# Kernel optimization log

Measured on AMD Instinct MI355X. Metric: run time of the kernel, lower is better.

Reference implementation:

```python
import jax, jax.numpy as jnp
import numpy as np

N_NODES = 100000
NEG_SLOPE = 0.2


def _gat_conv(x, edge_index, W, att_src, att_dst, bias):
    """Single-head PyG-style GATConv with self-loops.
    x: [N, F_in], edge_index: [2, E] (row 0 = src j, row 1 = dst i).
    """
    N = x.shape[0]
    h = x @ W  # [N, F_out]
    # add self-loops
    loop = jnp.arange(N, dtype=edge_index.dtype)
    src = jnp.concatenate([edge_index[0], loop])
    dst = jnp.concatenate([edge_index[1], loop])
    # per-node attention terms, gathered per edge
    a_s = h @ att_src  # [N]
    a_d = h @ att_dst  # [N]
    e = jax.nn.leaky_relu(a_s[src] + a_d[dst], NEG_SLOPE)  # [E+N]
    # segment softmax over incoming edges of each destination
    m = jax.ops.segment_max(e, dst, num_segments=N)  # [N]
    m = jnp.where(jnp.isfinite(m), m, 0.0)
    p = jnp.exp(e - m[dst])
    denom = jax.ops.segment_sum(p, dst, num_segments=N)  # [N], >0 due to self-loops
    alpha = p / denom[dst]  # [E+N]
    # scatter-aggregate weighted source features
    out = jax.ops.segment_sum(h[src] * alpha[:, None], dst, num_segments=N)
    return out + bias


def setup_inputs() -> dict:
    key = jax.random.key(0)
    ks = jax.random.split(key, 12)
    F_in, H, C = 128, 64, 40
    x = jax.random.normal(ks[0], (N_NODES, F_in), dtype=jnp.float32)
    edge_index = jax.random.randint(ks[1], (2, 1600000), 0, N_NODES, dtype=jnp.int64)
    s1 = 1.0 / np.sqrt(F_in)
    s2 = 1.0 / np.sqrt(H)
    return {
        "x": x,
        "edge_index": edge_index,
        "W1": jax.random.uniform(ks[2], (F_in, H), jnp.float32, -s1, s1),
        "att_src1": jax.random.uniform(ks[3], (H,), jnp.float32, -s2, s2),
        "att_dst1": jax.random.uniform(ks[4], (H,), jnp.float32, -s2, s2),
        "b1": jnp.zeros((H,), jnp.float32),
        "W2": jax.random.uniform(ks[5], (H, C), jnp.float32, -s2, s2),
        "att_src2": jax.random.uniform(ks[6], (C,), jnp.float32, -1.0 / np.sqrt(C), 1.0 / np.sqrt(C)),
        "att_dst2": jax.random.uniform(ks[7], (C,), jnp.float32, -1.0 / np.sqrt(C), 1.0 / np.sqrt(C)),
        "b2": jnp.zeros((C,), jnp.float32),
    }


def reference(x, edge_index, W1, att_src1, att_dst1, b1, W2, att_src2, att_dst2, b2):
    h = _gat_conv(x, edge_index, W1, att_src1, att_dst1, b1)
    h = jax.nn.relu(h)
    # dropout is identity in eval mode
    out = _gat_conv(h, edge_index, W2, att_src2, att_dst2, b2)
    return out
```

## Files before the change

### kernel.cpp

```cpp
#include <hip/hip_runtime.h>
#include <math.h>


#define NEG_SLOPE 0.2f
#define BIN_SHIFT 10
#define BIN_NODES 1024
#define MAXBINS   128
#define CAPB      17408
#define K1_CHUNK  4096
#define MAXDEG    128
#define AGG_STRIDE 132
#define XS_STRIDE 68

typedef _Float16 h4_t __attribute__((ext_vector_type(4)));

__device__ __forceinline__ float lrelu(float v) {
    return v > 0.f ? v : NEG_SLOPE * v;
}

__global__ __launch_bounds__(256) void bin_kernel(
    const int* __restrict__ src, const int* __restrict__ dst, int E, int nbins,
    int* __restrict__ bin_cursor, int* __restrict__ binned)
{
    __shared__ int hist[MAXBINS];
    __shared__ int base[MAXBINS];
    __shared__ int lcur[MAXBINS];
    const int tid = threadIdx.x;
    const int e0 = blockIdx.x * K1_CHUNK;

    if (tid < nbins) hist[tid] = 0;
    __syncthreads();

    for (int k = tid; k < K1_CHUNK; k += 256) {
        int e = e0 + k;
        if (e < E) atomicAdd(&hist[dst[e] >> BIN_SHIFT], 1);
    }
    __syncthreads();

    if (tid < nbins) {
        int c = hist[tid];
        base[tid] = (c > 0) ? atomicAdd(&bin_cursor[tid], c) : 0;
        lcur[tid] = 0;
    }
    __syncthreads();

    for (int k = tid; k < K1_CHUNK; k += 256) {
        int e = e0 + k;
        if (e < E) {
            int d = dst[e];
            int s = src[e];
            int b = d >> BIN_SHIFT;
            int o = atomicAdd(&lcur[b], 1);
            int pos = base[b] + o;
            if (pos < CAPB)
                binned[b * CAPB + pos] = (s << BIN_SHIFT) | (d & (BIN_NODES - 1));
        }
    }
}

__global__ __launch_bounds__(128) void scan_kernel(
    const int* __restrict__ bin_cursor, int* __restrict__ bin_base, int nbins)
{
    __shared__ int a[MAXBINS];
    const int tid = threadIdx.x;
    int v = (tid < nbins) ? min(bin_cursor[tid], CAPB) : 0;
    a[tid] = v;
    __syncthreads();
#pragma unroll
    for (int ofs = 1; ofs < 128; ofs <<= 1) {
        int t = (tid >= ofs) ? a[tid - ofs] : 0;
        __syncthreads();
        a[tid] += t;
        __syncthreads();
    }
    if (tid < nbins) bin_base[tid] = a[tid] - v;
}

__global__ __launch_bounds__(1024) void fine_kernel(
    const int* __restrict__ bin_cursor, const int* __restrict__ bin_base,
    const int* __restrict__ binned,
    int* __restrict__ csr, int* __restrict__ rowptr, int N, int nbins)
{
    __shared__ int a[BIN_NODES];
    __shared__ int cur[BIN_NODES];
    const int b = blockIdx.x;
    const int tid = threadIdx.x;

    const int cnt = min(bin_cursor[b], CAPB);
    const int binbase = bin_base[b];
    const int nn = min(BIN_NODES, N - b * BIN_NODES);
    const int* __restrict__ brec = binned + (long)b * CAPB;

    a[tid] = 0;
    __syncthreads();

    for (int k = tid; k < cnt; k += 1024) {
        atomicAdd(&a[brec[k] & (BIN_NODES - 1)], 1);
    }
    __syncthreads();

    int v = a[tid];
#pragma unroll
    for (int ofs = 1; ofs < BIN_NODES; ofs <<= 1) {
        int t = (tid >= ofs) ? a[tid - ofs] : 0;
        __syncthreads();
        a[tid] += t;
        __syncthreads();
    }
    const int excl = a[tid] - v;

    if (tid < nn) rowptr[b * BIN_NODES + tid] = binbase + excl;
    cur[tid] = binbase + excl;
    if (b == nbins - 1 && tid == 0) rowptr[N] = binbase + cnt;
    __syncthreads();

    for (int k = tid; k < cnt; k += 1024) {
        int rec = brec[k];
        int pos = atomicAdd(&cur[rec & (BIN_NODES - 1)], 1);
        csr[pos] = rec >> BIN_SHIFT;
    }
}

__global__ __launch_bounds__(256) void gemm1_kernel(
    const float* __restrict__ x, const float* __restrict__ W,
    const float* __restrict__ att_s, const float* __restrict__ att_d,
    _Float16* __restrict__ h, float* __restrict__ as_, float* __restrict__ ad_,
    int N)
{
    __shared__ float Ws[64 * 64];
    __shared__ float Xs[64 * XS_STRIDE];
    const int tid = threadIdx.x;
    const int cx = tid & 15;
    const int ry = tid >> 4;
    const long rowbase = (long)blockIdx.x * 64;
    const long gmax = (long)N * 32;

    float4 acc[4];
#pragma unroll
    for (int r = 0; r < 4; ++r) acc[r] = make_float4(0.f, 0.f, 0.f, 0.f);

    for (int kc = 0; kc < 2; ++kc) {
        __syncthreads();
        {
            const float4* W4 = (const float4*)W;
            float4* Ws4 = (float4*)Ws;
#pragma unroll
            for (int i = 0; i < 4; ++i)
                Ws4[tid + i * 256] = W4[kc * 1024 + tid + i * 256];
        }
        {
            const float4* X4 = (const float4*)x;
#pragma unroll
            for (int i = 0; i < 4; ++i) {
                int f = tid + i * 256;
                int row = f >> 4, c4 = f & 15;
                long gi = (rowbase + row) * 32 + kc * 16 + c4;
                float4 v = (gi < gmax) ? X4[gi] : make_float4(0.f, 0.f, 0.f, 0.f);
                *(float4*)&Xs[row * XS_STRIDE + c4 * 4] = v;
            }
        }
        __syncthreads();

#pragma unroll 4
        for (int k = 0; k < 64; k += 4) {
            float4 w0 = *(const float4*)&Ws[(k + 0) * 64 + cx * 4];
            float4 w1 = *(const float4*)&Ws[(k + 1) * 64 + cx * 4];
            float4 w2 = *(const float4*)&Ws[(k + 2) * 64 + cx * 4];
            float4 w3 = *(const float4*)&Ws[(k + 3) * 64 + cx * 4];
#pragma unroll
            for (int r = 0; r < 4; ++r) {
                float4 xv = *(const float4*)&Xs[(ry * 4 + r) * XS_STRIDE + k];
                acc[r].x += xv.x * w0.x + xv.y * w1.x + xv.z * w2.x + xv.w * w3.x;
                acc[r].y += xv.x * w0.y + xv.y * w1.y + xv.z * w2.y + xv.w * w3.y;
                acc[r].z += xv.x * w0.z + xv.y * w1.z + xv.z * w2.z + xv.w * w3.z;
                acc[r].w += xv.x * w0.w + xv.y * w1.w + xv.z * w2.w + xv.w * w3.w;
            }
        }
    }

    const float4 s4 = ((const float4*)att_s)[cx];
    const float4 d4 = ((const float4*)att_d)[cx];
#pragma unroll
    for (int r = 0; r < 4; ++r) {
        float ps = acc[r].x * s4.x + acc[r].y * s4.y + acc[r].z * s4.z + acc[r].w * s4.w;
        float pd = acc[r].x * d4.x + acc[r].y * d4.y + acc[r].z * d4.z + acc[r].w * d4.w;
#pragma unroll
        for (int off = 1; off < 16; off <<= 1) {
            ps += __shfl_xor(ps, off);
            pd += __shfl_xor(pd, off);
        }
        const long row = rowbase + ry * 4 + r;
        if (row < N) {
            h4_t hv;
            hv.x = (_Float16)acc[r].x; hv.y = (_Float16)acc[r].y;
            hv.z = (_Float16)acc[r].z; hv.w = (_Float16)acc[r].w;
            *(h4_t*)&h[row * 64 + cx * 4] = hv;
            if (cx == 0) { as_[row] = ps; ad_[row] = pd; }
        }
    }
}

__global__ __launch_bounds__(256) void gemm2_kernel(
    const float* __restrict__ hin, const float* __restrict__ W,
    const float* __restrict__ att_s, const float* __restrict__ att_d,
    _Float16* __restrict__ h2, float* __restrict__ as_, float* __restrict__ ad_,
    int N)
{
    __shared__ float Ws[64 * 40];
    __shared__ float Xs[64 * XS_STRIDE];
    const int tid = threadIdx.x;
    const int cx = tid & 15;
    const int ry = tid >> 4;
    const long rowbase = (long)blockIdx.x * 64;
    const bool act = (cx < 10);
    const int cq = act ? cx * 4 : 0;

    {
        const float4* W4 = (const float4*)W;
        float4* Ws4 = (float4*)Ws;
        Ws4[tid] = W4[tid];
        Ws4[tid + 256] = W4[tid + 256];
        if (tid < 128) Ws4[tid + 512] = W4[tid + 512];
    }
    {
        const float4* X4 = (const float4*)hin;
        const long gmax = (long)N * 16;
#pragma unroll
        for (int i = 0; i < 4; ++i) {
            int f = tid + i * 256;
            int row = f >> 4, c4 = f & 15;
            long gi = (rowbase + row) * 16 + c4;
            float4 v = (gi < gmax) ? X4[gi] : make_float4(0.f, 0.f, 0.f, 0.f);
            v.x = fmaxf(v.x, 0.f); v.y = fmaxf(v.y, 0.f);
            v.z = fmaxf(v.z, 0.f); v.w = fmaxf(v.w, 0.f);
            *(float4*)&Xs[row * XS_STRIDE + c4 * 4] = v;
        }
    }
    __syncthreads();

    float4 acc[4];
#pragma unroll
    for (int r = 0; r < 4; ++r) acc[r] = make_float4(0.f, 0.f, 0.f, 0.f);

#pragma unroll 4
    for (int k = 0; k < 64; k += 4) {
        float4 w0 = *(const float4*)&Ws[(k + 0) * 40 + cq];
        float4 w1 = *(const float4*)&Ws[(k + 1) * 40 + cq];
        float4 w2 = *(const float4*)&Ws[(k + 2) * 40 + cq];
        float4 w3 = *(const float4*)&Ws[(k + 3) * 40 + cq];
#pragma unroll
        for (int r = 0; r < 4; ++r) {
            float4 xv = *(const float4*)&Xs[(ry * 4 + r) * XS_STRIDE + k];
            acc[r].x += xv.x * w0.x + xv.y * w1.x + xv.z * w2.x + xv.w * w3.x;
            acc[r].y += xv.x * w0.y + xv.y * w1.y + xv.z * w2.y + xv.w * w3.y;
            acc[r].z += xv.x * w0.z + xv.y * w1.z + xv.z * w2.z + xv.w * w3.z;
            acc[r].w += xv.x * w0.w + xv.y * w1.w + xv.z * w2.w + xv.w * w3.w;
        }
    }

    const float4 s4 = act ? ((const float4*)att_s)[cx] : make_float4(0.f,0.f,0.f,0.f);
    const float4 d4 = act ? ((const float4*)att_d)[cx] : make_float4(0.f,0.f,0.f,0.f);
#pragma unroll
    for (int r = 0; r < 4; ++r) {
        float ps = act ? (acc[r].x * s4.x + acc[r].y * s4.y + acc[r].z * s4.z + acc[r].w * s4.w) : 0.f;
        float pd = act ? (acc[r].x * d4.x + acc[r].y * d4.y + acc[r].z * d4.z + acc[r].w * d4.w) : 0.f;
#pragma unroll
        for (int off = 1; off < 16; off <<= 1) {
            ps += __shfl_xor(ps, off);
            pd += __shfl_xor(pd, off);
        }
        const long row = rowbase + ry * 4 + r;
        if (row < N) {
            if (act) {
                h4_t hv;
                hv.x = (_Float16)acc[r].x; hv.y = (_Float16)acc[r].y;
                hv.z = (_Float16)acc[r].z; hv.w = (_Float16)acc[r].w;
                *(h4_t*)&h2[row * 40 + cq] = hv;
            }
            if (cx == 0) { as_[row] = ps; ad_[row] = pd; }
        }
    }
}

template<int F>
__global__ __launch_bounds__(256) void aggregate_kernel(
    const _Float16* __restrict__ h, const float* __restrict__ as_,
    const float* __restrict__ ad_, const int* __restrict__ rowptr,
    const int* __restrict__ csr, const float* __restrict__ bias,
    float* __restrict__ out, int N)
{
    __shared__ int   Ss[16 * AGG_STRIDE];
    __shared__ float Ps[16 * AGG_STRIDE];
    const int tid = threadIdx.x;
    const int dl  = tid >> 4;
    const int sub = tid & 15;
    const int i = blockIdx.x * 16 + dl;
    const bool alive = (i < N);

    int r0 = 0, deg = 0;
    if (alive) {
        r0 = rowptr[i];
        deg = rowptr[i + 1] - r0;
        if (deg > MAXDEG) deg = MAXDEG;
    }
    const float adi    = alive ? ad_[i] : 0.f;
    const float e_self = alive ? lrelu(as_[i] + adi) : 0.f;

    int*   __restrict__ sp = &Ss[dl * AGG_STRIDE];
    float* __restrict__ pp = &Ps[dl * AGG_STRIDE];

    float psum = 0.f;
    for (int c = sub; c < deg; c += 16) {
        int s = csr[r0 + c];
        float p = __expf(lrelu(as_[s] + adi));
        sp[c] = s;
        pp[c] = p;
        psum += p;
    }
#pragma unroll
    for (int off = 1; off < 16; off <<= 1) psum += __shfl_xor(psum, off);
    const float p_self = __expf(e_self);
    const float inv = 1.f / (psum + p_self);

    const bool act = (sub * 4 < F);
    const int  col = act ? sub * 4 : 0;
    float4 acc = make_float4(0.f, 0.f, 0.f, 0.f);

    int k = 0;
    for (; k + 4 <= deg; k += 4) {
        int   sA = sp[k],     sB = sp[k + 1], sC = sp[k + 2], sD = sp[k + 3];
        float pA = pp[k],     pB = pp[k + 1], pC = pp[k + 2], pD = pp[k + 3];
        if (act) {
            h4_t hA = *(const h4_t*)&h[(long)sA * F + col];
            h4_t hB = *(const h4_t*)&h[(long)sB * F + col];
            h4_t hC = *(const h4_t*)&h[(long)sC * F + col];
            h4_t hD = *(const h4_t*)&h[(long)sD * F + col];
            acc.x += (float)hA.x * pA + (float)hB.x * pB + (float)hC.x * pC + (float)hD.x * pD;
            acc.y += (float)hA.y * pA + (float)hB.y * pB + (float)hC.y * pC + (float)hD.y * pD;
            acc.z += (float)hA.z * pA + (float)hB.z * pB + (float)hC.z * pC + (float)hD.z * pD;
            acc.w += (float)hA.w * pA + (float)hB.w * pB + (float)hC.w * pC + (float)hD.w * pD;
        }
    }
    for (; k < deg; ++k) {
        int   s = sp[k];
        float p = pp[k];
        if (act) {
            h4_t hv = *(const h4_t*)&h[(long)s * F + col];
            acc.x += (float)hv.x * p; acc.y += (float)hv.y * p;
            acc.z += (float)hv.z * p; acc.w += (float)hv.w * p;
        }
    }

    if (alive && act) {
        h4_t hv = *(const h4_t*)&h[(long)i * F + col];
        float4 bv = *(const float4*)&bias[col];
        float4 o;
        o.x = (acc.x + (float)hv.x * p_self) * inv + bv.x;
        o.y = (acc.y + (float)hv.y * p_self) * inv + bv.y;
        o.z = (acc.z + (float)hv.z * p_self) * inv + bv.z;
        o.w = (acc.w + (float)hv.w * p_self) * inv + bv.w;
        *(float4*)&out[(long)i * F + col] = o;
    }
}

extern "C" void kernel_launch(void* const* d_in, const int* in_sizes, int n_in,
                              void* d_out, int out_size, void* d_ws, size_t ws_size,
                              hipStream_t stream) {
    const float* x    = (const float*)d_in[0];
    const int*   ei   = (const int*)d_in[1];
    const float* W1   = (const float*)d_in[2];
    const float* at_s1= (const float*)d_in[3];
    const float* at_d1= (const float*)d_in[4];
    const float* b1   = (const float*)d_in[5];
    const float* W2   = (const float*)d_in[6];
    const float* at_s2= (const float*)d_in[7];
    const float* at_d2= (const float*)d_in[8];
    const float* b2   = (const float*)d_in[9];
    float* out = (float*)d_out;

    const int N = in_sizes[0] / 128;
    const int E = in_sizes[1] / 2;
    const int nbins = (N + BIN_NODES - 1) >> BIN_SHIFT;

    char* p = (char*)d_ws;
    auto carve = [&](size_t bytes) -> void* {
        void* r = (void*)p;
        p += (bytes + 255) & ~(size_t)255;
        return r;
    };
    int*       bin_cursor = (int*)      carve((size_t)MAXBINS * 4);
    int*       bin_base   = (int*)      carve((size_t)MAXBINS * 4);
    int*       binned     = (int*)      carve((size_t)nbins * CAPB * 4);
    int*       csr        = (int*)      carve((size_t)E * 4);
    int*       rowptr     = (int*)      carve((size_t)(N + 1) * 4);
    _Float16*  h1         = (_Float16*) carve((size_t)N * 64 * 2);
    float*     agg1       = (float*)    carve((size_t)N * 64 * 4);
    _Float16*  h2         = (_Float16*) carve((size_t)N * 40 * 2);
    float*     asn        = (float*)    carve((size_t)N * 4);
    float*     adn        = (float*)    carve((size_t)N * 4);

    hipMemsetAsync(bin_cursor, 0, (size_t)MAXBINS * 4, stream);

    bin_kernel<<<(E + K1_CHUNK - 1) / K1_CHUNK, 256, 0, stream>>>(
        ei, ei + E, E, nbins, bin_cursor, binned);
    scan_kernel<<<1, 128, 0, stream>>>(bin_cursor, bin_base, nbins);
    fine_kernel<<<nbins, 1024, 0, stream>>>(bin_cursor, bin_base, binned, csr, rowptr, N, nbins);

    gemm1_kernel<<<(N + 63) / 64, 256, 0, stream>>>(x, W1, at_s1, at_d1, h1, asn, adn, N);
    aggregate_kernel<64><<<(N + 15) / 16, 256, 0, stream>>>(h1, asn, adn, rowptr, csr, b1, agg1, N);

    gemm2_kernel<<<(N + 63) / 64, 256, 0, stream>>>(agg1, W2, at_s2, at_d2, h2, asn, adn, N);
    aggregate_kernel<40><<<(N + 15) / 16, 256, 0, stream>>>(h2, asn, adn, rowptr, csr, b2, out, N);
}
```

Before: 271.4 us.

## Use fp16 MFMA for both GEMMs and store layer-1 output in fp16

Both dense projection kernels now use 32x32x16 fp16 MFMA instructions instead of scalar fp32 FMA loops. A new prep kernel transposes and converts W1 and W2 to fp16 for them. The attention dot products are reduced with wave shuffles plus shared-memory atomics. The first aggregation now writes its output in fp16, which halves the intermediate traffic read by the second GEMM. This costs precision in the matmul inputs and the hidden activations, and adds an extra small kernel launch.

```diff
diff --git a/kernel.cpp b/kernel.cpp
--- a/kernel.cpp
+++ b/kernel.cpp
@@ -10,12 +10,28 @@
 #define K1_CHUNK  4096
 #define MAXDEG    128
 #define AGG_STRIDE 132
-#define XS_STRIDE 68
 
 typedef _Float16 h4_t __attribute__((ext_vector_type(4)));
+typedef _Float16 h8_t __attribute__((ext_vector_type(8)));
+typedef float    f16x_t __attribute__((ext_vector_type(16)));
 
 __device__ __forceinline__ float lrelu(float v) {
     return v > 0.f ? v : NEG_SLOPE * v;
+}
+
+__global__ __launch_bounds__(256) void prep_kernel(
+    const float* __restrict__ W1, const float* __restrict__ W2,
+    _Float16* __restrict__ w1t, _Float16* __restrict__ w2t)
+{
+    const int tid = threadIdx.x;
+    for (int i = tid; i < 8192; i += 256) {
+        int n = i >> 7, k = i & 127;
+        w1t[i] = (_Float16)W1[k * 64 + n];
+    }
+    for (int i = tid; i < 4096; i += 256) {
+        int n = i >> 6, k = i & 63;
+        w2t[i] = (n < 40) ? (_Float16)W2[k * 40 + n] : (_Float16)0.f;
+    }
 }
 
 __global__ __launch_bounds__(256) void bin_kernel(
@@ -121,173 +137,176 @@
     }
 }
 
+#define XS1 136
 __global__ __launch_bounds__(256) void gemm1_kernel(
-    const float* __restrict__ x, const float* __restrict__ W,
+    const float* __restrict__ x, const _Float16* __restrict__ w1t,
     const float* __restrict__ att_s, const float* __restrict__ att_d,
     _Float16* __restrict__ h, float* __restrict__ as_, float* __restrict__ ad_,
     int N)
 {
-    __shared__ float Ws[64 * 64];
-    __shared__ float Xs[64 * XS_STRIDE];
-    const int tid = threadIdx.x;
-    const int cx = tid & 15;
-    const int ry = tid >> 4;
+    __shared__ __align__(16) _Float16 Xs[64 * XS1];
+    __shared__ __align__(16) _Float16 Wt[64 * XS1];
+    __shared__ float psrow[64], pdrow[64];
+    const int tid = threadIdx.x;
+    const int lane = tid & 63;
+    const int w = tid >> 6;
+    const int rh = w >> 1, ch = w & 1;
     const long rowbase = (long)blockIdx.x * 64;
-    const long gmax = (long)N * 32;
-
-    float4 acc[4];
-#pragma unroll
-    for (int r = 0; r < 4; ++r) acc[r] = make_float4(0.f, 0.f, 0.f, 0.f);
-
-    for (int kc = 0; kc < 2; ++kc) {
-        __syncthreads();
-        {
-            const float4* W4 = (const float4*)W;
-            float4* Ws4 = (float4*)Ws;
-#pragma unroll
-            for (int i = 0; i < 4; ++i)
-                Ws4[tid + i * 256] = W4[kc * 1024 + tid + i * 256];
-        }
-        {
-            const float4* X4 = (const float4*)x;
-#pragma unroll
-            for (int i = 0; i < 4; ++i) {
-                int f = tid + i * 256;
-                int row = f >> 4, c4 = f & 15;
-                long gi = (rowbase + row) * 32 + kc * 16 + c4;
-                float4 v = (gi < gmax) ? X4[gi] : make_float4(0.f, 0.f, 0.f, 0.f);
-                *(float4*)&Xs[row * XS_STRIDE + c4 * 4] = v;
-            }
-        }
-        __syncthreads();
-
-#pragma unroll 4
-        for (int k = 0; k < 64; k += 4) {
-            float4 w0 = *(const float4*)&Ws[(k + 0) * 64 + cx * 4];
-            float4 w1 = *(const float4*)&Ws[(k + 1) * 64 + cx * 4];
-            float4 w2 = *(const float4*)&Ws[(k + 2) * 64 + cx * 4];
-            float4 w3 = *(const float4*)&Ws[(k + 3) * 64 + cx * 4];
-#pragma unroll
-            for (int r = 0; r < 4; ++r) {
-                float4 xv = *(const float4*)&Xs[(ry * 4 + r) * XS_STRIDE + k];
-                acc[r].x += xv.x * w0.x + xv.y * w1.x + xv.z * w2.x + xv.w * w3.x;
-                acc[r].y += xv.x * w0.y + xv.y * w1.y + xv.z * w2.y + xv.w * w3.y;
-                acc[r].z += xv.x * w0.z + xv.y * w1.z + xv.z * w2.z + xv.w * w3.z;
-                acc[r].w += xv.x * w0.w + xv.y * w1.w + xv.z * w2.w + xv.w * w3.w;
-            }
-        }
-    }
-
-    const float4 s4 = ((const float4*)att_s)[cx];
-    const float4 d4 = ((const float4*)att_d)[cx];
-#pragma unroll
-    for (int r = 0; r < 4; ++r) {
-        float ps = acc[r].x * s4.x + acc[r].y * s4.y + acc[r].z * s4.z + acc[r].w * s4.w;
-        float pd = acc[r].x * d4.x + acc[r].y * d4.y + acc[r].z * d4.z + acc[r].w * d4.w;
-#pragma unroll
-        for (int off = 1; off < 16; off <<= 1) {
+
+    {
+        const int4* src = (const int4*)w1t;
+#pragma unroll
+        for (int i = 0; i < 4; ++i) {
+            int f = tid + i * 256;
+            int n = f >> 4, c = f & 15;
+            *(int4*)&Wt[n * XS1 + c * 8] = src[f];
+        }
+    }
+    {
+        const float4* X4 = (const float4*)x;
+        const long gmax = (long)N * 32;
+#pragma unroll
+        for (int i = 0; i < 8; ++i) {
+            int f = tid + i * 256;
+            int row = f >> 5, c4 = f & 31;
+            long gi = (rowbase + row) * 32 + c4;
+            float4 v = (gi < gmax) ? X4[gi] : make_float4(0.f, 0.f, 0.f, 0.f);
+            h4_t hv;
+            hv.x = (_Float16)v.x; hv.y = (_Float16)v.y;
+            hv.z = (_Float16)v.z; hv.w = (_Float16)v.w;
+            *(h4_t*)&Xs[row * XS1 + c4 * 4] = hv;
+        }
+    }
+    if (tid < 64) { psrow[tid] = 0.f; pdrow[tid] = 0.f; }
+    __syncthreads();
+
+    const int m = lane & 31, khalf = lane >> 5;
+    const _Float16* ax = &Xs[(rh * 32 + m) * XS1 + khalf * 8];
+    const _Float16* bx = &Wt[(ch * 32 + m) * XS1 + khalf * 8];
+
+    f16x_t acc = {};
+#pragma unroll
+    for (int kc = 0; kc < 8; ++kc) {
+        h8_t a = *(const h8_t*)(ax + kc * 16);
+        h8_t b = *(const h8_t*)(bx + kc * 16);
+        acc = __builtin_amdgcn_mfma_f32_32x32x16_f16(a, b, acc, 0, 0, 0);
+    }
+
+    const int col = ch * 32 + m;
+    const float asc = att_s[col], adc = att_d[col];
+#pragma unroll
+    for (int r = 0; r < 16; ++r) {
+        int rowl = (r & 3) + 8 * (r >> 2) + 4 * khalf;
+        long grow = rowbase + rh * 32 + rowl;
+        float v = acc[r];
+        if (grow < N) h[grow * 64 + col] = (_Float16)v;
+        float ps = v * asc, pd = v * adc;
+#pragma unroll
+        for (int off = 1; off < 32; off <<= 1) {
             ps += __shfl_xor(ps, off);
             pd += __shfl_xor(pd, off);
         }
-        const long row = rowbase + ry * 4 + r;
-        if (row < N) {
-            h4_t hv;
-            hv.x = (_Float16)acc[r].x; hv.y = (_Float16)acc[r].y;
-            hv.z = (_Float16)acc[r].z; hv.w = (_Float16)acc[r].w;
-            *(h4_t*)&h[row * 64 + cx * 4] = hv;
-            if (cx == 0) { as_[row] = ps; ad_[row] = pd; }
-        }
-    }
-}
-
+        if (m == 0) {
+            atomicAdd(&psrow[rh * 32 + rowl], ps);
+            atomicAdd(&pdrow[rh * 32 + rowl], pd);
+        }
+    }
+    __syncthreads();
+    if (tid < 64) {
+        long grow = rowbase + tid;
+        if (grow < N) { as_[grow] = psrow[tid]; ad_[grow] = pdrow[tid]; }
+    }
+}
+
+#define XS2 72
 __global__ __launch_bounds__(256) void gemm2_kernel(
-    const float* __restrict__ hin, const float* __restrict__ W,
+    const _Float16* __restrict__ hin, const _Float16* __restrict__ w2t,
     const float* __restrict__ att_s, const float* __restrict__ att_d,
     _Float16* __restrict__ h2, float* __restrict__ as_, float* __restrict__ ad_,
     int N)
 {
-    __shared__ float Ws[64 * 40];
-    __shared__ float Xs[64 * XS_STRIDE];
-    const int tid = threadIdx.x;
-    const int cx = tid & 15;
-    const int ry = tid >> 4;
+    __shared__ __align__(16) _Float16 Xs[64 * XS2];
+    __shared__ __align__(16) _Float16 Wt[64 * XS2];
+    __shared__ float psrow[64], pdrow[64];
+    const int tid = threadIdx.x;
+    const int lane = tid & 63;
+    const int w = tid >> 6;
+    const int rh = w >> 1, ch = w & 1;
     const long rowbase = (long)blockIdx.x * 64;
-    const bool act = (cx < 10);
-    const int cq = act ? cx * 4 : 0;
 
     {
-        const float4* W4 = (const float4*)W;
-        float4* Ws4 = (float4*)Ws;
-        Ws4[tid] = W4[tid];
-        Ws4[tid + 256] = W4[tid + 256];
-        if (tid < 128) Ws4[tid + 512] = W4[tid + 512];
+        const int4* src = (const int4*)w2t;
+#pragma unroll
+        for (int i = 0; i < 2; ++i) {
+            int f = tid + i * 256;
+            int n = f >> 3, c = f & 7;
+            *(int4*)&Wt[n * XS2 + c * 8] = src[f];
+        }
     }
     {
-        const float4* X4 = (const float4*)hin;
-        const long gmax = (long)N * 16;
-#pragma unroll
-        for (int i = 0; i < 4; ++i) {
+        const h8_t* X8 = (const h8_t*)hin;
+        const long gmax = (long)N * 8;
+#pragma unroll
+        for (int i = 0; i < 2; ++i) {
             int f = tid + i * 256;
-            int row = f >> 4, c4 = f & 15;
-            long gi = (rowbase + row) * 16 + c4;
-            float4 v = (gi < gmax) ? X4[gi] : make_float4(0.f, 0.f, 0.f, 0.f);
-            v.x = fmaxf(v.x, 0.f); v.y = fmaxf(v.y, 0.f);
-            v.z = fmaxf(v.z, 0.f); v.w = fmaxf(v.w, 0.f);
-            *(float4*)&Xs[row * XS_STRIDE + c4 * 4] = v;
-        }
-    }
-    __syncthreads();
-
-    float4 acc[4];
-#pragma unroll
-    for (int r = 0; r < 4; ++r) acc[r] = make_float4(0.f, 0.f, 0.f, 0.f);
-
-#pragma unroll 4
-    for (int k = 0; k < 64; k += 4) {
-        float4 w0 = *(const float4*)&Ws[(k + 0) * 40 + cq];
-        float4 w1 = *(const float4*)&Ws[(k + 1) * 40 + cq];
-        float4 w2 = *(const float4*)&Ws[(k + 2) * 40 + cq];
-        float4 w3 = *(const float4*)&Ws[(k + 3) * 40 + cq];
-#pragma unroll
-        for (int r = 0; r < 4; ++r) {
-            float4 xv = *(const float4*)&Xs[(ry * 4 + r) * XS_STRIDE + k];
-            acc[r].x += xv.x * w0.x + xv.y * w1.x + xv.z * w2.x + xv.w * w3.x;
-            acc[r].y += xv.x * w0.y + xv.y * w1.y + xv.z * w2.y + xv.w * w3.y;
-            acc[r].z += xv.x * w0.z + xv.y * w1.z + xv.z * w2.z + xv.w * w3.z;
-            acc[r].w += xv.x * w0.w + xv.y * w1.w + xv.z * w2.w + xv.w * w3.w;
-        }
-    }
-
-    const float4 s4 = act ? ((const float4*)att_s)[cx] : make_float4(0.f,0.f,0.f,0.f);
-    const float4 d4 = act ? ((const float4*)att_d)[cx] : make_float4(0.f,0.f,0.f,0.f);
-#pragma unroll
-    for (int r = 0; r < 4; ++r) {
-        float ps = act ? (acc[r].x * s4.x + acc[r].y * s4.y + acc[r].z * s4.z + acc[r].w * s4.w) : 0.f;
-        float pd = act ? (acc[r].x * d4.x + acc[r].y * d4.y + acc[r].z * d4.z + acc[r].w * d4.w) : 0.f;
-#pragma unroll
-        for (int off = 1; off < 16; off <<= 1) {
+            int row = f >> 3, c = f & 7;
+            long gi = (rowbase + row) * 8 + c;
+            h8_t v = {};
+            if (gi < gmax) v = X8[gi];
+#pragma unroll
+            for (int j = 0; j < 8; ++j) v[j] = (v[j] > (_Float16)0.f) ? v[j] : (_Float16)0.f;
+            *(h8_t*)&Xs[row * XS2 + c * 8] = v;
+        }
+    }
+    if (tid < 64) { psrow[tid] = 0.f; pdrow[tid] = 0.f; }
+    __syncthreads();
+
+    const int m = lane & 31, khalf = lane >> 5;
+    const _Float16* ax = &Xs[(rh * 32 + m) * XS2 + khalf * 8];
+    const _Float16* bx = &Wt[(ch * 32 + m) * XS2 + khalf * 8];
+
+    f16x_t acc = {};
+#pragma unroll
+    for (int kc = 0; kc < 4; ++kc) {
+        h8_t a = *(const h8_t*)(ax + kc * 16);
+        h8_t b = *(const h8_t*)(bx + kc * 16);
+        acc = __builtin_amdgcn_mfma_f32_32x32x16_f16(a, b, acc, 0, 0, 0);
+    }
+
+    const int col = ch * 32 + m;
+    const bool cval = (col < 40);
+    const float asc = cval ? att_s[col] : 0.f;
+    const float adc = cval ? att_d[col] : 0.f;
+#pragma unroll
+    for (int r = 0; r < 16; ++r) {
+        int rowl = (r & 3) + 8 * (r >> 2) + 4 * khalf;
+        long grow = rowbase + rh * 32 + rowl;
+        float v = acc[r];
+        if (cval && grow < N) h2[grow * 40 + col] = (_Float16)v;
+        float ps = v * asc, pd = v * adc;
+#pragma unroll
+        for (int off = 1; off < 32; off <<= 1) {
             ps += __shfl_xor(ps, off);
             pd += __shfl_xor(pd, off);
         }
-        const long row = rowbase + ry * 4 + r;
-        if (row < N) {
-            if (act) {
-                h4_t hv;
-                hv.x = (_Float16)acc[r].x; hv.y = (_Float16)acc[r].y;
-                hv.z = (_Float16)acc[r].z; hv.w = (_Float16)acc[r].w;
-                *(h4_t*)&h2[row * 40 + cq] = hv;
-            }
-            if (cx == 0) { as_[row] = ps; ad_[row] = pd; }
-        }
-    }
-}
-
-template<int F>
+        if (m == 0) {
+            atomicAdd(&psrow[rh * 32 + rowl], ps);
+            atomicAdd(&pdrow[rh * 32 + rowl], pd);
+        }
+    }
+    __syncthreads();
+    if (tid < 64) {
+        long grow = rowbase + tid;
+        if (grow < N) { as_[grow] = psrow[tid]; ad_[grow] = pdrow[tid]; }
+    }
+}
+
+template<int F, typename OT>
 __global__ __launch_bounds__(256) void aggregate_kernel(
     const _Float16* __restrict__ h, const float* __restrict__ as_,
     const float* __restrict__ ad_, const int* __restrict__ rowptr,
     const int* __restrict__ csr, const float* __restrict__ bias,
-    float* __restrict__ out, int N)
+    OT* __restrict__ out, int N)
 {
     __shared__ int   Ss[16 * AGG_STRIDE];
     __shared__ float Ps[16 * AGG_STRIDE];
@@ -354,12 +373,19 @@
     if (alive && act) {
         h4_t hv = *(const h4_t*)&h[(long)i * F + col];
         float4 bv = *(const float4*)&bias[col];
-        float4 o;
-        o.x = (acc.x + (float)hv.x * p_self) * inv + bv.x;
-        o.y = (acc.y + (float)hv.y * p_self) * inv + bv.y;
-        o.z = (acc.z + (float)hv.z * p_self) * inv + bv.z;
-        o.w = (acc.w + (float)hv.w * p_self) * inv + bv.w;
-        *(float4*)&out[(long)i * F + col] = o;
+        float ox = (acc.x + (float)hv.x * p_self) * inv + bv.x;
+        float oy = (acc.y + (float)hv.y * p_self) * inv + bv.y;
+        float oz = (acc.z + (float)hv.z * p_self) * inv + bv.z;
+        float ow = (acc.w + (float)hv.w * p_self) * inv + bv.w;
+        if constexpr (sizeof(OT) == 4) {
+            float4 o = make_float4(ox, oy, oz, ow);
+            *(float4*)&out[(long)i * F + col] = o;
+        } else {
+            h4_t o;
+            o.x = (_Float16)ox; o.y = (_Float16)oy;
+            o.z = (_Float16)oz; o.w = (_Float16)ow;
+            *(h4_t*)&out[(long)i * F + col] = o;
+        }
     }
 }
 
@@ -393,22 +419,27 @@
     int*       binned     = (int*)      carve((size_t)nbins * CAPB * 4);
     int*       csr        = (int*)      carve((size_t)E * 4);
     int*       rowptr     = (int*)      carve((size_t)(N + 1) * 4);
+    _Float16*  w1t        = (_Float16*) carve((size_t)8192 * 2);
+    _Float16*  w2t        = (_Float16*) carve((size_t)4096 * 2);
     _Float16*  h1         = (_Float16*) carve((size_t)N * 64 * 2);
-    float*     agg1       = (float*)    carve((size_t)N * 64 * 4);
+    _Float16*  agg1h      = (_Float16*) carve((size_t)N * 64 * 2);
     _Float16*  h2         = (_Float16*) carve((size_t)N * 40 * 2);
     float*     asn        = (float*)    carve((size_t)N * 4);
     float*     adn        = (float*)    carve((size_t)N * 4);
 
     hipMemsetAsync(bin_cursor, 0, (size_t)MAXBINS * 4, stream);
 
+    prep_kernel<<<1, 256, 0, stream>>>(W1, W2, w1t, w2t);
     bin_kernel<<<(E + K1_CHUNK - 1) / K1_CHUNK, 256, 0, stream>>>(
         ei, ei + E, E, nbins, bin_cursor, binned);
     scan_kernel<<<1, 128, 0, stream>>>(bin_cursor, bin_base, nbins);
     fine_kernel<<<nbins, 1024, 0, stream>>>(bin_cursor, bin_base, binned, csr, rowptr, N, nbins);
 
-    gemm1_kernel<<<(N + 63) / 64, 256, 0, stream>>>(x, W1, at_s1, at_d1, h1, asn, adn, N);
-    aggregate_kernel<64><<<(N + 15) / 16, 256, 0, stream>>>(h1, asn, adn, rowptr, csr, b1, agg1, N);
-
-    gemm2_kernel<<<(N + 63) / 64, 256, 0, stream>>>(agg1, W2, at_s2, at_d2, h2, asn, adn, N);
-    aggregate_kernel<40><<<(N + 15) / 16, 256, 0, stream>>>(h2, asn, adn, rowptr, csr, b2, out, N);
-}
+    gemm1_kernel<<<(N + 63) / 64, 256, 0, stream>>>(x, w1t, at_s1, at_d1, h1, asn, adn, N);
+    aggregate_kernel<64, _Float16><<<(N + 15) / 16, 256, 0, stream>>>(
+        h1, asn, adn, rowptr, csr, b1, agg1h, N);
+
+    gemm2_kernel<<<(N + 63) / 64, 256, 0, stream>>>(agg1h, w2t, at_s2, at_d2, h2, asn, adn, N);
+    aggregate_kernel<40, float><<<(N + 15) / 16, 256, 0, stream>>>(
+        h2, asn, adn, rowptr, csr, b2, out, N);
+}
```

Result: no change. 271.6 us (+0.1%).
